# Kernel tuning notes

Measured on AMD Instinct MI355X. Metric: run time of the kernel, lower is better.

The kernel has to match this reference:

```python
import jax, jax.numpy as jnp
import numpy as np

N_EMBD = 1024
N_HEAD = 16
HEAD_DIM = N_EMBD // N_HEAD
B, T = 2, 2048


def setup_inputs() -> dict:
    key = jax.random.key(0)
    ks = jax.random.split(key, 9)
    s = 1.0 / np.sqrt(N_EMBD)
    return {
        "x": jax.random.normal(ks[0], (B, T, N_EMBD), dtype=jnp.float32),
        "Wq": jax.random.normal(ks[1], (N_EMBD, N_EMBD), dtype=jnp.float32) * s,
        "bq": jax.random.normal(ks[2], (N_EMBD,), dtype=jnp.float32) * s,
        "Wk": jax.random.normal(ks[3], (N_EMBD, N_EMBD), dtype=jnp.float32) * s,
        "bk": jax.random.normal(ks[4], (N_EMBD,), dtype=jnp.float32) * s,
        "Wv": jax.random.normal(ks[5], (N_EMBD, N_EMBD), dtype=jnp.float32) * s,
        "bv": jax.random.normal(ks[6], (N_EMBD,), dtype=jnp.float32) * s,
        "Wp": jax.random.normal(ks[7], (N_EMBD, N_EMBD), dtype=jnp.float32) * s,
        "bp": jax.random.normal(ks[8], (N_EMBD,), dtype=jnp.float32) * s,
    }


def reference(x, Wq, bq, Wk, bk, Wv, bv, Wp, bp):
    b, t, c = x.shape
    # torch Linear: y = x @ W.T + b
    def proj(W, bias):
        y = jnp.einsum('btc,oc->bto', x, W) + bias
        return y.reshape(b, t, N_HEAD, HEAD_DIM).transpose(0, 2, 1, 3)  # [B,H,T,D]

    q = proj(Wq, bq)
    k = proj(Wk, bk)
    v = proj(Wv, bv)

    scale = 1.0 / np.sqrt(HEAD_DIM).astype(np.float32)
    scores = jnp.einsum('bhqd,bhkd->bhqk', q, k) * scale  # [B,H,T,T]
    causal = jnp.tril(jnp.ones((t, t), dtype=bool))
    scores = jnp.where(causal[None, None], scores, jnp.float32(-jnp.inf))
    attn = jax.nn.softmax(scores, axis=-1)
    out = jnp.einsum('bhqk,bhkd->bhqd', attn, v)  # [B,H,T,D]
    out = out.transpose(0, 2, 1, 3).reshape(b, t, c)
    out = jnp.einsum('btc,oc->bto', out, Wp) + bp
    return out
```

## Files before the change

kernel.cpp:

```cpp
#include <hip/hip_runtime.h>
#include <hip/hip_bf16.h>

#define TT 2048
#define MM 4096

typedef __attribute__((ext_vector_type(8))) short bf16x8;
typedef __attribute__((ext_vector_type(4))) float f32x4;

__device__ inline short f2bf(float f){
  union { float f; unsigned u; } x; x.f = f;
  unsigned r = x.u + 0x7FFFu + ((x.u >> 16) & 1u);
  return (short)(r >> 16);
}
__device__ inline int pk2bf(float a, float b){
  __hip_bfloat162 h2 = __float22bfloat162_rn(make_float2(a, b));
  return *(int*)&h2;
}

__device__ inline void async16(const void* g, void* l){
  __builtin_amdgcn_global_load_lds((const __attribute__((address_space(1))) void*)g,
                                   (__attribute__((address_space(3))) void*)l, 16, 0, 0);
}

__global__ void cvt_all(const float* __restrict__ x,
                        const float* __restrict__ Wq, const float* __restrict__ Wk,
                        const float* __restrict__ Wv, const float* __restrict__ Wp,
                        short* __restrict__ xb, short* __restrict__ Wqb, short* __restrict__ Wkb,
                        short* __restrict__ Wvb, short* __restrict__ Wpb){
  int b = blockIdx.x;
  const float* in; short* out; int base;
  if (b < 4096)      { in = x;  out = xb;  base = b; }
  else if (b < 5120) { in = Wq; out = Wqb; base = b - 4096; }
  else if (b < 6144) { in = Wk; out = Wkb; base = b - 5120; }
  else if (b < 7168) { in = Wv; out = Wvb; base = b - 6144; }
  else               { in = Wp; out = Wpb; base = b - 7168; }
  int i = base * 256 + threadIdx.x;
  float4 v = ((const float4*)in)[i];
  short4 o;
  o.x = f2bf(v.x); o.y = f2bf(v.y); o.z = f2bf(v.z); o.w = f2bf(v.w);
  ((short4*)out)[i] = o;
}

__device__ inline void gemm_core(const short* __restrict__ A, const short* __restrict__ Wm,
                                 short* As, short* Bs, int m0, int n0,
                                 int tid, int wm, int wn, int quad, int lr,
                                 f32x4 acc[4][4])
{
  const int prow = tid >> 2, pcol = (tid & 3) << 3;
  const short* Ap0 = A  + (size_t)(m0 + prow) * 1024 + pcol;
  const short* Ap1 = A  + (size_t)(m0 + prow + 64) * 1024 + pcol;
  const short* Bp0 = Wm + (size_t)(n0 + prow) * 1024 + pcol;
  const short* Bp1 = Wm + (size_t)(n0 + prow + 64) * 1024 + pcol;
  for (int kt = 0; kt < 16; ++kt){
    const int kk = kt * 64;
#pragma unroll
    for (int pn = 0; pn < 2; ++pn){
      async16(Ap0 + kk + pn*32, As + pn*4096 + (size_t)tid * 8);
      async16(Ap1 + kk + pn*32, As + pn*4096 + (size_t)(tid + 256) * 8);
      async16(Bp0 + kk + pn*32, Bs + pn*4096 + (size_t)tid * 8);
      async16(Bp1 + kk + pn*32, Bs + pn*4096 + (size_t)(tid + 256) * 8);
    }
    __syncthreads();
#pragma unroll
    for (int ks = 0; ks < 2; ++ks){
      bf16x8 aF[4], bF[4];
#pragma unroll
      for (int mt = 0; mt < 4; ++mt) aF[mt] = *(const bf16x8*)(As + ks*4096 + (wm*64 + mt*16 + lr)*32 + quad*8);
#pragma unroll
      for (int nt = 0; nt < 4; ++nt) bF[nt] = *(const bf16x8*)(Bs + ks*4096 + (wn*64 + nt*16 + lr)*32 + quad*8);
#pragma unroll
      for (int mt = 0; mt < 4; ++mt)
#pragma unroll
        for (int nt = 0; nt < 4; ++nt)
          acc[mt][nt] = __builtin_amdgcn_mfma_f32_16x16x32_bf16(aF[mt], bF[nt], acc[mt][nt], 0, 0, 0);
    }
    __syncthreads();
  }
}

__launch_bounds__(256, 3)
__global__ void gemm_qkv(const short* __restrict__ A,
                         const short* __restrict__ W0, const short* __restrict__ W1, const short* __restrict__ W2,
                         const float* __restrict__ b0, const float* __restrict__ b1, const float* __restrict__ b2,
                         short* __restrict__ Qo, short* __restrict__ Ko, short* __restrict__ Vt)
{
  __shared__ __align__(16) short smem[16384];
  short* As = smem;
  short* Bs = smem + 8192;
  const int z = blockIdx.z;
  const short* Wm   = (z == 0) ? W0 : ((z == 1) ? W1 : W2);
  const float* bias = (z == 0) ? b0 : ((z == 1) ? b1 : b2);
  const int tid = threadIdx.x;
  const int lane = tid & 63, wave = tid >> 6;
  const int wm = wave >> 1, wn = wave & 1;
  const int quad = lane >> 4, lr = lane & 15;
  const int m0 = blockIdx.y * 128, n0 = blockIdx.x * 128;

  f32x4 acc[4][4];
#pragma unroll
  for (int i = 0; i < 4; ++i)
#pragma unroll
    for (int j = 0; j < 4; ++j)
#pragma unroll
      for (int r = 0; r < 4; ++r) acc[i][j][r] = 0.f;

  gemm_core(A, Wm, As, Bs, m0, n0, tid, wm, wn, quad, lr, acc);

  const float qscale = 0.125f * 1.4426950408889634f;
  const int bB = m0 >> 11, t0 = m0 & 2047;

  if (z == 2){
#pragma unroll
    for (int nh = 0; nh < 2; ++nh){
      __syncthreads();
      if (wn == nh){
#pragma unroll
        for (int nt = 0; nt < 4; ++nt){
          int n = n0 + wn*64 + nt*16 + lr;
          float bv = bias[n];
          int n_l = nt*16 + lr;
#pragma unroll
          for (int mt = 0; mt < 4; ++mt)
#pragma unroll
            for (int r = 0; r < 4; ++r){
              int m_l = wm*64 + mt*16 + quad*4 + r;
              smem[n_l*136 + m_l] = f2bf(acc[mt][nt][r] + bv);
            }
        }
      }
      __syncthreads();
#pragma unroll
      for (int i = 0; i < 4; ++i){
        int c = tid + i*256;
        int rowN = c >> 4, ch = c & 15;
        int4 v = *(const int4*)(smem + rowN*136 + ch*8);
        int n = n0 + nh*64 + rowN;
        int hH = n >> 6, d = n & 63;
        *(int4*)(Vt + ((size_t)((bB<<4) + hH)*64 + d)*2048 + t0 + ch*8) = v;
      }
    }
    return;
  }

  short* dst = (z == 0) ? Qo : Ko;
#pragma unroll
  for (int nh = 0; nh < 2; ++nh){
    __syncthreads();
    if (wn == nh){
#pragma unroll
      for (int nt = 0; nt < 4; ++nt){
        int n_l = nt*16 + lr;
        float bv = bias[n0 + nh*64 + n_l];
#pragma unroll
        for (int mt = 0; mt < 4; ++mt){
#pragma unroll
          for (int r = 0; r < 4; ++r){
            int m_l = wm*64 + mt*16 + quad*4 + r;
            float v = acc[mt][nt][r] + bv;
            if (z == 0) v *= qscale;
            smem[m_l*72 + n_l] = f2bf(v);
          }
        }
      }
    }
    __syncthreads();
    const int hH = (n0 + nh*64) >> 6;
    short* dhead = dst + (size_t)((bB<<4) + hH) * 2048 * 64;
#pragma unroll
    for (int i = 0; i < 4; ++i){
      int c = tid + i*256;
      int rowm = c >> 3, ch = (c & 7) << 3;
      int4 v = *(const int4*)(smem + rowm*72 + ch);
      *(int4*)(dhead + (size_t)(t0 + rowm)*64 + ch) = v;
    }
  }
}

__launch_bounds__(256, 2)
__global__ void gemm_proj(const short* __restrict__ A, const short* __restrict__ Wm,
                          const float* __restrict__ bias, float* __restrict__ out)
{
  __shared__ __align__(16) short As[2*4096];
  __shared__ __align__(16) short Bs[2*2048];
  const int tid = threadIdx.x;
  const int lane = tid & 63, wave = tid >> 6;
  const int quad = lane >> 4, lr = lane & 15;
  const int m0 = blockIdx.y * 128, n0 = blockIdx.x * 64;

  const int prow = tid >> 2, pcol = (tid & 3) << 3;
  const short* Ap0 = A  + (size_t)(m0 + prow) * 1024 + pcol;
  const short* Ap1 = A  + (size_t)(m0 + prow + 64) * 1024 + pcol;
  const short* Bp0 = Wm + (size_t)(n0 + (tid >> 2)) * 1024 + pcol;

  f32x4 acc[2][4];
#pragma unroll
  for (int i = 0; i < 2; ++i)
#pragma unroll
    for (int j = 0; j < 4; ++j)
#pragma unroll
      for (int r = 0; r < 4; ++r) acc[i][j][r] = 0.f;

  for (int kt = 0; kt < 16; ++kt){
    const int kk = kt * 64;
#pragma unroll
    for (int pn = 0; pn < 2; ++pn){
      async16(Ap0 + kk + pn*32, As + pn*4096 + (size_t)tid * 8);
      async16(Ap1 + kk + pn*32, As + pn*4096 + (size_t)(tid + 256) * 8);
      async16(Bp0 + kk + pn*32, Bs + pn*2048 + (size_t)tid * 8);
    }
    __syncthreads();
#pragma unroll
    for (int ks = 0; ks < 2; ++ks){
      bf16x8 aF[2], bF[4];
#pragma unroll
      for (int mt = 0; mt < 2; ++mt) aF[mt] = *(const bf16x8*)(As + ks*4096 + (wave*32 + mt*16 + lr)*32 + quad*8);
#pragma unroll
      for (int nt = 0; nt < 4; ++nt) bF[nt] = *(const bf16x8*)(Bs + ks*2048 + (nt*16 + lr)*32 + quad*8);
#pragma unroll
      for (int mt = 0; mt < 2; ++mt)
#pragma unroll
        for (int nt = 0; nt < 4; ++nt)
          acc[mt][nt] = __builtin_amdgcn_mfma_f32_16x16x32_bf16(aF[mt], bF[nt], acc[mt][nt], 0, 0, 0);
    }
    __syncthreads();
  }

#pragma unroll
  for (int nt = 0; nt < 4; ++nt){
    int n = n0 + nt*16 + lr;
    float bv = bias[n];
#pragma unroll
    for (int mt = 0; mt < 2; ++mt){
      int mBase = m0 + wave*32 + mt*16 + quad*4;
#pragma unroll
      for (int r = 0; r < 4; ++r){
        int m = mBase + r;
        out[(size_t)m * 1024 + n] = acc[mt][nt][r] + bv;
      }
    }
  }
}

__device__ __constant__ int slice_tbl[24] = {
  14352, 30736,     2,
  31760, 26638,  2052,
  12302, 27534,  4102,
  28687, 20491,  6152,
  29647, 19082, 16393,
  24589, 10252, 16969,
  25421, 21195,  8202,
  22540, 23308, 18442
};

__launch_bounds__(256, 3)
__global__ void attn_kernel(const short* __restrict__ Q, const short* __restrict__ K,
                            const short* __restrict__ Vt, short* __restrict__ AO,
                            float* __restrict__ Opart, float* __restrict__ Lpart)
{
  __shared__ __align__(16) short Ks[2][4096];
  __shared__ __align__(16) short Vs[2][4096];
  __shared__ __align__(16) short Ps[8192];
  const int tid = threadIdx.x, lane = tid & 63, wave = tid >> 6;
  const int quad = lane >> 4, lr = lane & 15;
  const int bid = blockIdx.x;
  const int a = (bid >> 5) & 7;
  const int hb = bid & 31;
  const int j = bid >> 8;
  const int e = slice_tbl[a*3 + j];
  const int qb = e >> 11, kv_s = (e >> 6) & 31, kvn = e & 63;
  const bool split = (kvn != 2*qb + 2);
  const int half = (kv_s != 0) ? 1 : 0;
  const int bidx = hb >> 4, h = hb & 15;
  const int wq0 = qb * 128 + wave * 32;
  const short* Qh = Q  + (size_t)hb * TT * 64;
  const short* Kh = K  + (size_t)hb * TT * 64;
  const short* Vh = Vt + (size_t)hb * 64 * TT;
  short* Pw = Ps + wave * 2048;

  const int srow = tid >> 3;
  const int ssw  = (tid & 7) ^ (srow & 7);
  const short* Kp0 = Kh + (size_t)srow * 64 + ssw * 8;
  const short* Vp0 = Vh + (size_t)srow * TT + ssw * 8;

  bf16x8 qf[2][2];
#pragma unroll
  for (int g = 0; g < 2; ++g)
#pragma unroll
    for (int ks = 0; ks < 2; ++ks)
      qf[g][ks] = *(const bf16x8*)(Qh + (size_t)(wq0 + g*16 + lr) * 64 + ks*32 + quad*8);

  const int lsw0 = (((0*4 + quad) ^ (lr & 7)) << 3);
  const int lsw1 = (((1*4 + quad) ^ (lr & 7)) << 3);
  const int qh2 = quad >> 1, qlo = (quad & 1) << 2;

  f32x4 acc_o[2][4], l_acc[2];
#pragma unroll
  for (int g = 0; g < 2; ++g){
#pragma unroll
    for (int r = 0; r < 4; ++r) l_acc[g][r] = 0.f;
#pragma unroll
    for (int dt = 0; dt < 4; ++dt)
#pragma unroll
      for (int r = 0; r < 4; ++r) acc_o[g][dt][r] = 0.f;
  }

  const short one_bf = (short)0x3F80;
  const bf16x8 onesf = { one_bf, one_bf, one_bf, one_bf, one_bf, one_bf, one_bf, one_bf };

  const int kv_e = kv_s + kvn;
  const int qtw = wq0 >> 6;
  {
    const short* kp = Kp0 + (size_t)kv_s * 4096;
    const short* vp = Vp0 + kv_s * 64;
    async16(kp,          &Ks[0][(size_t)tid * 8]);
    async16(kp + 32*64,  &Ks[0][(size_t)(tid + 256) * 8]);
    async16(vp,          &Vs[0][(size_t)tid * 8]);
    async16(vp + 32*TT,  &Vs[0][(size_t)(tid + 256) * 8]);
  }

  const short* kp_n = Kp0 + (size_t)(kv_s + 1) * 4096;
  const short* vp_n = Vp0 + (kv_s + 1) * 64;

  int cur = 0;
  for (int kv = kv_s; kv < kv_e; ++kv){
    const int kv0 = kv * 64;
    __syncthreads();
    if (kv + 1 < kv_e){
      const int nb = cur ^ 1;
      async16(kp_n,          &Ks[nb][(size_t)tid * 8]);
      async16(kp_n + 32*64,  &Ks[nb][(size_t)(tid + 256) * 8]);
      async16(vp_n,          &Vs[nb][(size_t)tid * 8]);
      async16(vp_n + 32*TT,  &Vs[nb][(size_t)(tid + 256) * 8]);
      kp_n += 4096; vp_n += 64;
    }
    if (kv0 <= wq0 + 31){
      f32x4 s4[2][4];
#pragma unroll
      for (int g = 0; g < 2; ++g)
#pragma unroll
        for (int nt = 0; nt < 4; ++nt)
#pragma unroll
          for (int r = 0; r < 4; ++r) s4[g][nt][r] = 0.f;
#pragma unroll
      for (int nt = 0; nt < 4; ++nt){
        bf16x8 kf0 = *(const bf16x8*)(&Ks[cur][(nt*16 + lr)*64 + lsw0]);
        bf16x8 kf1 = *(const bf16x8*)(&Ks[cur][(nt*16 + lr)*64 + lsw1]);
#pragma unroll
        for (int g = 0; g < 2; ++g){
          s4[g][nt] = __builtin_amdgcn_mfma_f32_16x16x32_bf16(kf0, qf[g][0], s4[g][nt], 0, 0, 0);
          s4[g][nt] = __builtin_amdgcn_mfma_f32_16x16x32_bf16(kf1, qf[g][1], s4[g][nt], 0, 0, 0);
        }
      }

      if (kv == qtw){
#pragma unroll
        for (int g = 0; g < 2; ++g){
          const int qglob = wq0 + g*16 + lr;
          short* Pg = Pw + g*1024;
#pragma unroll
          for (int nt = 0; nt < 4; ++nt){
            const int keyb = kv0 + nt*16 + quad*4;
            float pv[4];
#pragma unroll
            for (int r = 0; r < 4; ++r){
              float v = exp2f(s4[g][nt][r]);
              if (keyb + r > qglob) v = 0.f;
              pv[r] = v;
            }
            int2 w;
            w.x = pk2bf(pv[0], pv[1]);
            w.y = pk2bf(pv[2], pv[3]);
            const int gg = nt*2 + qh2;
            *(int2*)(Pg + lr*64 + ((gg ^ (lr & 7)) << 3) + qlo) = w;
          }
        }
      } else {
#pragma unroll
        for (int g = 0; g < 2; ++g){
          short* Pg = Pw + g*1024;
#pragma unroll
          for (int nt = 0; nt < 4; ++nt){
            int2 w;
            w.x = pk2bf(exp2f(s4[g][nt][0]), exp2f(s4[g][nt][1]));
            w.y = pk2bf(exp2f(s4[g][nt][2]), exp2f(s4[g][nt][3]));
            const int gg = nt*2 + qh2;
            *(int2*)(Pg + lr*64 + ((gg ^ (lr & 7)) << 3) + qlo) = w;
          }
        }
      }

#pragma unroll
      for (int ks = 0; ks < 2; ++ks){
        const int lsw = ks ? lsw1 : lsw0;
        bf16x8 ptf0 = *(const bf16x8*)(Pw + lr*64 + lsw);
        bf16x8 ptf1 = *(const bf16x8*)(Pw + 1024 + lr*64 + lsw);
        l_acc[0] = __builtin_amdgcn_mfma_f32_16x16x32_bf16(onesf, ptf0, l_acc[0], 0, 0, 0);
        l_acc[1] = __builtin_amdgcn_mfma_f32_16x16x32_bf16(onesf, ptf1, l_acc[1], 0, 0, 0);
#pragma unroll
        for (int dt = 0; dt < 4; ++dt){
          bf16x8 vf = *(const bf16x8*)(&Vs[cur][(dt*16 + lr)*64 + lsw]);
          acc_o[0][dt] = __builtin_amdgcn_mfma_f32_16x16x32_bf16(vf, ptf0, acc_o[0][dt], 0, 0, 0);
          acc_o[1][dt] = __builtin_amdgcn_mfma_f32_16x16x32_bf16(vf, ptf1, acc_o[1][dt], 0, 0, 0);
        }
      }
    }
    cur ^= 1;
  }

  if (split){
    const int p = (((hb << 3) | (qb - 8)) << 1) + half;
    float* Op = Opart + (size_t)p * 8192;
#pragma unroll
    for (int g = 0; g < 2; ++g){
      const int q_l = wave*32 + g*16 + lr;
#pragma unroll
      for (int dt = 0; dt < 4; ++dt)
        *(f32x4*)(Op + q_l*64 + dt*16 + quad*4) = acc_o[g][dt];
      if (lane < 16) Lpart[p*128 + wave*32 + g*16 + lane] = l_acc[g][0];
    }
    return;
  }

#pragma unroll
  for (int g = 0; g < 2; ++g){
    short* Pg = Pw + g*1024;
    const float inv = __builtin_amdgcn_rcpf(l_acc[g][0]);
#pragma unroll
    for (int dt = 0; dt < 4; ++dt){
      int2 w;
      w.x = pk2bf(acc_o[g][dt][0] * inv, acc_o[g][dt][1] * inv);
      w.y = pk2bf(acc_o[g][dt][2] * inv, acc_o[g][dt][3] * inv);
      const int gg = dt*2 + qh2;
      *(int2*)(Pg + lr*64 + ((gg ^ (lr & 7)) << 3) + qlo) = w;
    }
#pragma unroll
    for (int i = 0; i < 2; ++i){
      int c = lane + i*64;
      int row = c >> 3, ch = c & 7;
      int4 v = *(const int4*)(Pg + row*64 + ((ch ^ (row & 7)) << 3));
      *(int4*)(AO + (size_t)(bidx*2048 + wq0 + g*16 + row)*1024 + h*64 + ch*8) = v;
    }
  }
}

__global__ void attn_combine(const float* __restrict__ Opart, const float* __restrict__ Lpart,
                             short* __restrict__ AO)
{
  const int gid = blockIdx.x * 256 + threadIdx.x;
  const int row = gid >> 4, dq = (gid & 15) << 2;
  const int hb = row >> 10, band = (row >> 7) & 7, r = row & 127;
  const int p = ((hb << 3) | band) << 1;
  const f32x4 a = *(const f32x4*)(Opart + (size_t)p*8192 + r*64 + dq);
  const f32x4 b = *(const f32x4*)(Opart + (size_t)(p+1)*8192 + r*64 + dq);
  const float l = Lpart[p*128 + r] + Lpart[(p+1)*128 + r];
  const float inv = __builtin_amdgcn_rcpf(l);
  int2 w;
  w.x = pk2bf((a[0]+b[0])*inv, (a[1]+b[1])*inv);
  w.y = pk2bf((a[2]+b[2])*inv, (a[3]+b[3])*inv);
  const int t = (8 + band)*128 + r;
  const int bidx = hb >> 4, h = hb & 15;
  *(int2*)(AO + (size_t)(bidx*2048 + t)*1024 + h*64 + dq) = w;
}

extern "C" void kernel_launch(void* const* d_in, const int* in_sizes, int n_in,
                              void* d_out, int out_size, void* d_ws, size_t ws_size,
                              hipStream_t stream)
{
  const float* x  = (const float*)d_in[0];
  const float* Wq = (const float*)d_in[1];
  const float* bq = (const float*)d_in[2];
  const float* Wk = (const float*)d_in[3];
  const float* bk = (const float*)d_in[4];
  const float* Wv = (const float*)d_in[5];
  const float* bv = (const float*)d_in[6];
  const float* Wp = (const float*)d_in[7];
  const float* bp = (const float*)d_in[8];
  float* out = (float*)d_out;

  char* ws = (char*)d_ws;
  const size_t MB = 1024ull * 1024ull;
  short* Qb  = (short*)(ws + 0);
  short* Kb  = (short*)(ws + 8*MB);
  short* Vtb = (short*)(ws + 16*MB);
  short* AOb = (short*)(ws + 24*MB);
  short* xb  = (short*)(ws + 24*MB);
  short* Wqb = (short*)(ws + 32*MB);
  short* Wkb = (short*)(ws + 34*MB);
  short* Wvb = (short*)(ws + 36*MB);
  short* Wpb = (short*)(ws + 38*MB);
  float* Opart = (float*)(ws + 40*MB);
  float* Lpart = (float*)(ws + 56*MB);

  cvt_all<<<8192, 256, 0, stream>>>(x, Wq, Wk, Wv, Wp, xb, Wqb, Wkb, Wvb, Wpb);
  gemm_qkv<<<dim3(8, 32, 3), 256, 0, stream>>>(xb, Wqb, Wkb, Wvb, bq, bk, bv, Qb, Kb, Vtb);
  attn_kernel<<<768, 256, 0, stream>>>(Qb, Kb, Vtb, AOb, Opart, Lpart);
  attn_combine<<<2048, 256, 0, stream>>>(Opart, Lpart, AOb);
  gemm_proj<<<dim3(16, 32), 256, 0, stream>>>(AOb, Wpb, bp, out);
}
```

Measured before the change: 182.7 us.

## Double-buffer LDS tiles in QKV and projection GEMMs to overlap loads with MFMA

Turns the single-buffered K-loop in both GEMM kernels into a two-stage ping-pong pipeline. The next K tile is issued with async global-to-LDS loads right after the barrier, while MFMAs run on the current buffer, and the trailing barrier is dropped. This aims to hide global load latency behind compute. The cost is double the LDS use and launch bounds on gemm_qkv lowered from 3 to 2, which lowers occupancy.

Result: slower. 202.2 us (+10.7%).

```diff
diff --git a/kernel.cpp b/kernel.cpp
--- a/kernel.cpp
+++ b/kernel.cpp
@@ -41,6 +41,18 @@
   ((short4*)out)[i] = o;
 }
 
+__device__ inline void stage_qkv(const short* Ap0, const short* Ap1,
+                                 const short* Bp0, const short* Bp1,
+                                 int kk, short* As, short* Bs, int tid){
+#pragma unroll
+  for (int pn = 0; pn < 2; ++pn){
+    async16(Ap0 + kk + pn*32, As + pn*4096 + (size_t)tid * 8);
+    async16(Ap1 + kk + pn*32, As + pn*4096 + (size_t)(tid + 256) * 8);
+    async16(Bp0 + kk + pn*32, Bs + pn*4096 + (size_t)tid * 8);
+    async16(Bp1 + kk + pn*32, Bs + pn*4096 + (size_t)(tid + 256) * 8);
+  }
+}
+
 __device__ inline void gemm_core(const short* __restrict__ A, const short* __restrict__ Wm,
                                  short* As, short* Bs, int m0, int n0,
                                  int tid, int wm, int wn, int quad, int lr,
@@ -48,45 +60,42 @@
 {
   const int prow = tid >> 2, pcol = (tid & 3) << 3;
   const short* Ap0 = A  + (size_t)(m0 + prow) * 1024 + pcol;
-  const short* Ap1 = A  + (size_t)(m0 + prow + 64) * 1024 + pcol;
+  const short* Ap1 = Ap0 + 64 * 1024;
   const short* Bp0 = Wm + (size_t)(n0 + prow) * 1024 + pcol;
-  const short* Bp1 = Wm + (size_t)(n0 + prow + 64) * 1024 + pcol;
+  const short* Bp1 = Bp0 + 64 * 1024;
+
+  stage_qkv(Ap0, Ap1, Bp0, Bp1, 0, As, Bs, tid);
+  int cur = 0;
   for (int kt = 0; kt < 16; ++kt){
-    const int kk = kt * 64;
-#pragma unroll
-    for (int pn = 0; pn < 2; ++pn){
-      async16(Ap0 + kk + pn*32, As + pn*4096 + (size_t)tid * 8);
-      async16(Ap1 + kk + pn*32, As + pn*4096 + (size_t)(tid + 256) * 8);
-      async16(Bp0 + kk + pn*32, Bs + pn*4096 + (size_t)tid * 8);
-      async16(Bp1 + kk + pn*32, Bs + pn*4096 + (size_t)(tid + 256) * 8);
-    }
     __syncthreads();
+    if (kt + 1 < 16)
+      stage_qkv(Ap0, Ap1, Bp0, Bp1, (kt+1)*64, As + (cur^1)*8192, Bs + (cur^1)*8192, tid);
 #pragma unroll
     for (int ks = 0; ks < 2; ++ks){
       bf16x8 aF[4], bF[4];
 #pragma unroll
-      for (int mt = 0; mt < 4; ++mt) aF[mt] = *(const bf16x8*)(As + ks*4096 + (wm*64 + mt*16 + lr)*32 + quad*8);
-#pragma unroll
-      for (int nt = 0; nt < 4; ++nt) bF[nt] = *(const bf16x8*)(Bs + ks*4096 + (wn*64 + nt*16 + lr)*32 + quad*8);
+      for (int mt = 0; mt < 4; ++mt) aF[mt] = *(const bf16x8*)(As + cur*8192 + ks*4096 + (wm*64 + mt*16 + lr)*32 + quad*8);
+#pragma unroll
+      for (int nt = 0; nt < 4; ++nt) bF[nt] = *(const bf16x8*)(Bs + cur*8192 + ks*4096 + (wn*64 + nt*16 + lr)*32 + quad*8);
 #pragma unroll
       for (int mt = 0; mt < 4; ++mt)
 #pragma unroll
         for (int nt = 0; nt < 4; ++nt)
           acc[mt][nt] = __builtin_amdgcn_mfma_f32_16x16x32_bf16(aF[mt], bF[nt], acc[mt][nt], 0, 0, 0);
     }
-    __syncthreads();
-  }
-}
-
-__launch_bounds__(256, 3)
+    cur ^= 1;
+  }
+}
+
+__launch_bounds__(256, 2)
 __global__ void gemm_qkv(const short* __restrict__ A,
                          const short* __restrict__ W0, const short* __restrict__ W1, const short* __restrict__ W2,
                          const float* __restrict__ b0, const float* __restrict__ b1, const float* __restrict__ b2,
                          short* __restrict__ Qo, short* __restrict__ Ko, short* __restrict__ Vt)
 {
-  __shared__ __align__(16) short smem[16384];
-  short* As = smem;
-  short* Bs = smem + 8192;
+  __shared__ __align__(16) short As[2*8192];
+  __shared__ __align__(16) short Bs[2*8192];
+  short* smem = As;
   const int z = blockIdx.z;
   const short* Wm   = (z == 0) ? W0 : ((z == 1) ? W1 : W2);
   const float* bias = (z == 0) ? b0 : ((z == 1) ? b1 : b2);
@@ -180,8 +189,8 @@
 __global__ void gemm_proj(const short* __restrict__ A, const short* __restrict__ Wm,
                           const float* __restrict__ bias, float* __restrict__ out)
 {
-  __shared__ __align__(16) short As[2*4096];
-  __shared__ __align__(16) short Bs[2*2048];
+  __shared__ __align__(16) short As[2*8192];
+  __shared__ __align__(16) short Bs[2*4096];
   const int tid = threadIdx.x;
   const int lane = tid & 63, wave = tid >> 6;
   const int quad = lane >> 4, lr = lane & 15;
@@ -189,8 +198,8 @@
 
   const int prow = tid >> 2, pcol = (tid & 3) << 3;
   const short* Ap0 = A  + (size_t)(m0 + prow) * 1024 + pcol;
-  const short* Ap1 = A  + (size_t)(m0 + prow + 64) * 1024 + pcol;
-  const short* Bp0 = Wm + (size_t)(n0 + (tid >> 2)) * 1024 + pcol;
+  const short* Ap1 = Ap0 + 64 * 1024;
+  const short* Bp0 = Wm + (size_t)(n0 + prow) * 1024 + pcol;
 
   f32x4 acc[2][4];
 #pragma unroll
@@ -200,29 +209,40 @@
 #pragma unroll
       for (int r = 0; r < 4; ++r) acc[i][j][r] = 0.f;
 
+#pragma unroll
+  for (int pn = 0; pn < 2; ++pn){
+    async16(Ap0 + pn*32, As + pn*4096 + (size_t)tid * 8);
+    async16(Ap1 + pn*32, As + pn*4096 + (size_t)(tid + 256) * 8);
+    async16(Bp0 + pn*32, Bs + pn*2048 + (size_t)tid * 8);
+  }
+  int cur = 0;
   for (int kt = 0; kt < 16; ++kt){
-    const int kk = kt * 64;
-#pragma unroll
-    for (int pn = 0; pn < 2; ++pn){
-      async16(Ap0 + kk + pn*32, As + pn*4096 + (size_t)tid * 8);
-      async16(Ap1 + kk + pn*32, As + pn*4096 + (size_t)(tid + 256) * 8);
-      async16(Bp0 + kk + pn*32, Bs + pn*2048 + (size_t)tid * 8);
-    }
     __syncthreads();
+    if (kt + 1 < 16){
+      const int kk = (kt + 1) * 64;
+      short* Ad = As + (cur^1)*8192;
+      short* Bd = Bs + (cur^1)*4096;
+#pragma unroll
+      for (int pn = 0; pn < 2; ++pn){
+        async16(Ap0 + kk + pn*32, Ad + pn*4096 + (size_t)tid * 8);
+        async16(Ap1 + kk + pn*32, Ad + pn*4096 + (size_t)(tid + 256) * 8);
+        async16(Bp0 + kk + pn*32, Bd + pn*2048 + (size_t)tid * 8);
+      }
+    }
 #pragma unroll
     for (int ks = 0; ks < 2; ++ks){
       bf16x8 aF[2], bF[4];
 #pragma unroll
-      for (int mt = 0; mt < 2; ++mt) aF[mt] = *(const bf16x8*)(As + ks*4096 + (wave*32 + mt*16 + lr)*32 + quad*8);
-#pragma unroll
-      for (int nt = 0; nt < 4; ++nt) bF[nt] = *(const bf16x8*)(Bs + ks*2048 + (nt*16 + lr)*32 + quad*8);
+      for (int mt = 0; mt < 2; ++mt) aF[mt] = *(const bf16x8*)(As + cur*8192 + ks*4096 + (wave*32 + mt*16 + lr)*32 + quad*8);
+#pragma unroll
+      for (int nt = 0; nt < 4; ++nt) bF[nt] = *(const bf16x8*)(Bs + cur*4096 + ks*2048 + (nt*16 + lr)*32 + quad*8);
 #pragma unroll
       for (int mt = 0; mt < 2; ++mt)
 #pragma unroll
         for (int nt = 0; nt < 4; ++nt)
           acc[mt][nt] = __builtin_amdgcn_mfma_f32_16x16x32_bf16(aF[mt], bF[nt], acc[mt][nt], 0, 0, 0);
     }
-    __syncthreads();
+    cur ^= 1;
   }
 
 #pragma unroll
```

## Use 128x128 split-K tiles for output projection with separate combine kernel

Applied to the files above, without the earlier changes.

The output projection GEMM now reuses the shared 128x128 gemm_core and splits K into two halves across blockIdx.z. Each half writes fp32 partials to a workspace buffer, and a new proj_combine kernel sums the halves and adds the bias. The larger tile raises data reuse while split-K keeps 512 blocks in flight. In exchange it adds an extra launch and 32 MB of fp32 partial traffic (written, then read back).

After: 188.6 us. 3.2% more time.

```diff
diff --git a/kernel.cpp b/kernel.cpp
--- a/kernel.cpp
+++ b/kernel.cpp
@@ -42,16 +42,16 @@
 }
 
 __device__ inline void gemm_core(const short* __restrict__ A, const short* __restrict__ Wm,
-                                 short* As, short* Bs, int m0, int n0,
+                                 short* As, short* Bs, int m0, int n0, int k0, int nkt,
                                  int tid, int wm, int wn, int quad, int lr,
                                  f32x4 acc[4][4])
 {
   const int prow = tid >> 2, pcol = (tid & 3) << 3;
-  const short* Ap0 = A  + (size_t)(m0 + prow) * 1024 + pcol;
-  const short* Ap1 = A  + (size_t)(m0 + prow + 64) * 1024 + pcol;
-  const short* Bp0 = Wm + (size_t)(n0 + prow) * 1024 + pcol;
-  const short* Bp1 = Wm + (size_t)(n0 + prow + 64) * 1024 + pcol;
-  for (int kt = 0; kt < 16; ++kt){
+  const short* Ap0 = A  + (size_t)(m0 + prow) * 1024 + k0 + pcol;
+  const short* Ap1 = Ap0 + 64 * 1024;
+  const short* Bp0 = Wm + (size_t)(n0 + prow) * 1024 + k0 + pcol;
+  const short* Bp1 = Bp0 + 64 * 1024;
+  for (int kt = 0; kt < nkt; ++kt){
     const int kk = kt * 64;
 #pragma unroll
     for (int pn = 0; pn < 2; ++pn){
@@ -104,7 +104,7 @@
 #pragma unroll
       for (int r = 0; r < 4; ++r) acc[i][j][r] = 0.f;
 
-  gemm_core(A, Wm, As, Bs, m0, n0, tid, wm, wn, quad, lr, acc);
+  gemm_core(A, Wm, As, Bs, m0, n0, 0, 16, tid, wm, wn, quad, lr, acc);
 
   const float qscale = 0.125f * 1.4426950408889634f;
   const int bB = m0 >> 11, t0 = m0 & 2047;
@@ -176,69 +176,53 @@
   }
 }
 
-__launch_bounds__(256, 2)
+__launch_bounds__(256, 3)
 __global__ void gemm_proj(const short* __restrict__ A, const short* __restrict__ Wm,
-                          const float* __restrict__ bias, float* __restrict__ out)
-{
-  __shared__ __align__(16) short As[2*4096];
-  __shared__ __align__(16) short Bs[2*2048];
+                          float* __restrict__ Pp)
+{
+  __shared__ __align__(16) short smem[16384];
   const int tid = threadIdx.x;
   const int lane = tid & 63, wave = tid >> 6;
+  const int wm = wave >> 1, wn = wave & 1;
   const int quad = lane >> 4, lr = lane & 15;
-  const int m0 = blockIdx.y * 128, n0 = blockIdx.x * 64;
-
-  const int prow = tid >> 2, pcol = (tid & 3) << 3;
-  const short* Ap0 = A  + (size_t)(m0 + prow) * 1024 + pcol;
-  const short* Ap1 = A  + (size_t)(m0 + prow + 64) * 1024 + pcol;
-  const short* Bp0 = Wm + (size_t)(n0 + (tid >> 2)) * 1024 + pcol;
-
-  f32x4 acc[2][4];
-#pragma unroll
-  for (int i = 0; i < 2; ++i)
+  const int m0 = blockIdx.y * 128, n0 = blockIdx.x * 128;
+  const int k0 = blockIdx.z * 512;
+
+  f32x4 acc[4][4];
+#pragma unroll
+  for (int i = 0; i < 4; ++i)
 #pragma unroll
     for (int j = 0; j < 4; ++j)
 #pragma unroll
       for (int r = 0; r < 4; ++r) acc[i][j][r] = 0.f;
 
-  for (int kt = 0; kt < 16; ++kt){
-    const int kk = kt * 64;
-#pragma unroll
-    for (int pn = 0; pn < 2; ++pn){
-      async16(Ap0 + kk + pn*32, As + pn*4096 + (size_t)tid * 8);
-      async16(Ap1 + kk + pn*32, As + pn*4096 + (size_t)(tid + 256) * 8);
-      async16(Bp0 + kk + pn*32, Bs + pn*2048 + (size_t)tid * 8);
-    }
-    __syncthreads();
-#pragma unroll
-    for (int ks = 0; ks < 2; ++ks){
-      bf16x8 aF[2], bF[4];
-#pragma unroll
-      for (int mt = 0; mt < 2; ++mt) aF[mt] = *(const bf16x8*)(As + ks*4096 + (wave*32 + mt*16 + lr)*32 + quad*8);
-#pragma unroll
-      for (int nt = 0; nt < 4; ++nt) bF[nt] = *(const bf16x8*)(Bs + ks*2048 + (nt*16 + lr)*32 + quad*8);
-#pragma unroll
-      for (int mt = 0; mt < 2; ++mt)
-#pragma unroll
-        for (int nt = 0; nt < 4; ++nt)
-          acc[mt][nt] = __builtin_amdgcn_mfma_f32_16x16x32_bf16(aF[mt], bF[nt], acc[mt][nt], 0, 0, 0);
-    }
-    __syncthreads();
-  }
-
+  gemm_core(A, Wm, smem, smem + 8192, m0, n0, k0, 8, tid, wm, wn, quad, lr, acc);
+
+  float* Op = Pp + (size_t)blockIdx.z * 4194304;
 #pragma unroll
   for (int nt = 0; nt < 4; ++nt){
-    int n = n0 + nt*16 + lr;
-    float bv = bias[n];
-#pragma unroll
-    for (int mt = 0; mt < 2; ++mt){
-      int mBase = m0 + wave*32 + mt*16 + quad*4;
-#pragma unroll
-      for (int r = 0; r < 4; ++r){
-        int m = mBase + r;
-        out[(size_t)m * 1024 + n] = acc[mt][nt][r] + bv;
-      }
-    }
-  }
+    int n = n0 + wn*64 + nt*16 + lr;
+#pragma unroll
+    for (int mt = 0; mt < 4; ++mt){
+      int mBase = m0 + wm*64 + mt*16 + quad*4;
+#pragma unroll
+      for (int r = 0; r < 4; ++r)
+        Op[(size_t)(mBase + r) * 1024 + n] = acc[mt][nt][r];
+    }
+  }
+}
+
+__global__ void proj_combine(const float* __restrict__ Pp, const float* __restrict__ bias,
+                             float* __restrict__ out)
+{
+  const int gid = blockIdx.x * 256 + threadIdx.x;
+  const f32x4 a = *(const f32x4*)(Pp + (size_t)gid * 4);
+  const f32x4 b = *(const f32x4*)(Pp + 4194304 + (size_t)gid * 4);
+  const f32x4 bv = *(const f32x4*)(bias + ((gid << 2) & 1023));
+  f32x4 o;
+#pragma unroll
+  for (int r = 0; r < 4; ++r) o[r] = a[r] + b[r] + bv[r];
+  *(f32x4*)(out + (size_t)gid * 4) = o;
 }
 
 __device__ __constant__ int slice_tbl[24] = {
@@ -490,10 +474,12 @@
   short* Wpb = (short*)(ws + 38*MB);
   float* Opart = (float*)(ws + 40*MB);
   float* Lpart = (float*)(ws + 56*MB);
+  float* Pproj = (float*)(ws + 64*MB);
 
   cvt_all<<<8192, 256, 0, stream>>>(x, Wq, Wk, Wv, Wp, xb, Wqb, Wkb, Wvb, Wpb);
   gemm_qkv<<<dim3(8, 32, 3), 256, 0, stream>>>(xb, Wqb, Wkb, Wvb, bq, bk, bv, Qb, Kb, Vtb);
   attn_kernel<<<768, 256, 0, stream>>>(Qb, Kb, Vtb, AOb, Opart, Lpart);
   attn_combine<<<2048, 256, 0, stream>>>(Opart, Lpart, AOb);
-  gemm_proj<<<dim3(16, 32), 256, 0, stream>>>(AOb, Wpb, bp, out);
-}
+  gemm_proj<<<dim3(8, 32, 2), 256, 0, stream>>>(AOb, Wpb, Pproj);
+  proj_combine<<<4096, 256, 0, stream>>>(Pproj, bp, out);
+}
```
